# Performance work log

Hardware: AMD Instinct MI355X
Metric: run time of the kernel (lower is better)

The kernel has to match this reference:

```python
import jax, jax.numpy as jnp
import numpy as np

B, LQ, LK, D = 8, 1024, 4096, 1024


def setup_inputs() -> dict:
    key = jax.random.key(0)
    k1, k2, k3, k4, k5, k6 = jax.random.split(key, 6)
    s = 1.0 / np.sqrt(D)
    return {
        "T": jax.random.normal(k1, (B, LQ, D), dtype=jnp.float32),
        "S": jax.random.normal(k2, (B, LK, D), dtype=jnp.float32),
        "Wq": jax.random.uniform(k3, (D, D), jnp.float32, -s, s),
        "Wk": jax.random.uniform(k4, (D, D), jnp.float32, -s, s),
        "Wv": jax.random.uniform(k5, (D, D), jnp.float32, -s, s),
        "Wo": jax.random.uniform(k6, (D, D), jnp.float32, -s, s),
    }


def reference(T, S, Wq, Wk, Wv, Wo):
    # Linear layers: y = x @ W.T (torch nn.Linear convention), bias=False
    q = jnp.einsum('bqd,ed->bqe', T, Wq)          # [B, LQ, D]
    k = jnp.einsum('bkd,ed->bke', S, Wk)          # [B, LK, D]
    v = jnp.einsum('bkd,ed->bke', S, Wv)          # [B, LK, D]
    scale = jnp.asarray(D, q.dtype) ** -0.5        # hidden_dim ** -0.5 (single head)
    attn = jnp.einsum('bqe,bke->bqk', q, k) * scale  # [B, LQ, LK]
    attn = jax.nn.softmax(attn, axis=-1)
    out = jnp.einsum('bqk,bke->bqe', attn, v)      # [B, LQ, D]
    return jnp.einsum('bqe,fe->bqf', out, Wo)      # output projection
```

## Files before the change

kernel.cpp:

```cpp
#include <hip/hip_runtime.h>
#include <stdint.h>

typedef __bf16 bf16;
typedef __bf16 bf16x8 __attribute__((ext_vector_type(8)));
typedef float f32x4 __attribute__((ext_vector_type(4)));

__device__ __forceinline__ void gload_lds16(const void* g, void* l) {
    __builtin_amdgcn_global_load_lds(
        (const __attribute__((address_space(1))) unsigned int*)g,
        (__attribute__((address_space(3))) unsigned int*)l, 16, 0, 0);
}

#define BAR()    asm volatile("s_barrier" ::: "memory")
#define WAITV(N) asm volatile("s_waitcnt vmcnt(" #N ")" ::: "memory")

template<int OMODE>
__global__ __launch_bounds__(512, 2)
void gemm256(const bf16* __restrict__ A, const bf16* __restrict__ B,
             void* __restrict__ Cv, int K, int N,
             long batchA, long batchB, long batchC, float alpha,
             int nbx, int nby, int GC)
{
    __shared__ __align__(16) bf16 lds[2][4][8192];

    const int nwg  = gridDim.x;
    const int orig = blockIdx.x;
    const int q8   = nwg >> 3, r8 = nwg & 7;
    const int xcd  = orig & 7, lid = orig >> 3;
    const int p    = (xcd < r8 ? xcd * (q8 + 1) : r8 * (q8 + 1) + (xcd - r8) * q8) + lid;
    const int perb = nbx * nby;
    const int z    = p / perb;
    const int pb   = p - z * perb;
    const int sw   = nby * GC;
    const int st   = pb / sw;
    const int rem  = pb - st * sw;
    const int by   = rem / GC;
    const int bx   = st * GC + (rem - by * GC);

    const long rowb = (long)by << 8;
    const long colb = (long)bx << 8;

    const int t  = threadIdx.x;
    const int l  = t & 63;
    const int w  = t >> 6;
    const int wm = w >> 2;
    const int wn = w & 3;

    const int sL   = (t * 16) ^ (((t >> 3) & 3) << 4);
    const int srow = sL >> 6;
    const int sk   = (sL & 63) >> 1;
    const bf16* Ab = A + (long)z * batchA;
    const bf16* Bb = B + (long)z * batchB;
    const bf16* gA = Ab + (rowb + srow) * (long)K + sk;
    const bf16* gB = Bb + (colb + srow) * (long)K + sk;
    const long rstep = 128L * K;
    const int  d0 = t * 8, d1 = t * 8 + 4096;

    const int xl    = ((l >> 1) & 3) << 4;
    const int aBase = ((wm * 128 + (l & 15)) * 64 + ((l >> 4) << 4)) ^ xl;
    const int bBase = ((wn * 64  + (l & 15)) * 64 + ((l >> 4) << 4)) ^ xl;

    f32x4 acc[8][4] = {};
    bf16x8 av[4], bv[4];

#define STG(S, R, G, KOFF) do { \
    const bf16* _g = (G) + (KOFF); \
    gload_lds16(_g,         &lds[S][R][d0]); \
    gload_lds16(_g + rstep, &lds[S][R][d1]); \
  } while (0)

#define RD(S, R, OFF) (*(const bf16x8*)((const char*)&lds[S][R][0] + (OFF)))

#define MM(MB) \
    __builtin_amdgcn_s_setprio(1); \
    _Pragma("unroll") for (int mi = 0; mi < 4; ++mi) \
      _Pragma("unroll") for (int nj = 0; nj < 4; ++nj) \
        acc[MB + mi][nj] = __builtin_amdgcn_mfma_f32_16x16x32_bf16(av[mi], bv[nj], acc[MB + mi][nj], 0, 0, 0); \
    __builtin_amdgcn_s_setprio(0);

#define PH1(S, STGX) { \
    _Pragma("unroll") for (int nj = 0; nj < 4; ++nj) bv[nj] = RD(S, 2, bBase + nj * 1024); \
    _Pragma("unroll") for (int mi = 0; mi < 4; ++mi) av[mi] = RD(S, 0, aBase + mi * 1024); \
    STGX; BAR(); MM(0) BAR(); }

#define PH2(S, STGX) { \
    _Pragma("unroll") for (int mi = 0; mi < 4; ++mi) av[mi] = RD(S, 0, aBase + 4096 + mi * 1024); \
    STGX; BAR(); MM(4) BAR(); }

#define PH3(S, STGX) { \
    _Pragma("unroll") for (int nj = 0; nj < 4; ++nj) bv[nj] = RD(S, 3, bBase + nj * 1024); \
    _Pragma("unroll") for (int mi = 0; mi < 4; ++mi) av[mi] = RD(S, 1, aBase + mi * 1024); \
    STGX; BAR(); MM(0) BAR(); }

#define PH4(S, STGX, WT) { \
    _Pragma("unroll") for (int mi = 0; mi < 4; ++mi) av[mi] = RD(S, 1, aBase + 4096 + mi * 1024); \
    STGX; BAR(); MM(4) WT; BAR(); }

    STG(0, 0, gA, 0);
    STG(0, 1, gA, 32);
    STG(0, 2, gB, 0);
    STG(0, 3, gB, 32);
    STG(1, 2, gB, 64);
    STG(1, 0, gA, 64);
    STG(1, 3, gB, 96);
    WAITV(6);
    BAR();

    const int NI = K >> 7;
    for (int i = 0; i < NI - 1; ++i) {
        const int kb = i << 7;
        const int kn = kb + 128;
        PH1(0, STG(1, 1, gA, kb + 96));
        PH2(0, STG(0, 2, gB, kn));
        PH3(0, STG(0, 0, gA, kn));
        PH4(0, STG(0, 3, gB, kn + 32), WAITV(6));
        PH1(1, STG(0, 1, gA, kn + 32));
        PH2(1, STG(1, 2, gB, kn + 64));
        PH3(1, STG(1, 0, gA, kn + 64));
        PH4(1, STG(1, 3, gB, kn + 96), WAITV(6));
    }
    {
        const int kb = (NI - 1) << 7;
        PH1(0, STG(1, 1, gA, kb + 96));
        PH2(0, );
        PH3(0, );
        PH4(0, , WAITV(0));
        PH1(1, );
        PH2(1, );
        PH3(1, );
        PH4(1, , );
    }
#undef STG
#undef RD
#undef MM
#undef PH1
#undef PH2
#undef PH3
#undef PH4

    const int r0 = (l >> 4) << 2;

    if constexpr (OMODE == 2) {
        const long cb0 = colb + wn * 64 + (l & 15);
        const long rb0 = rowb + wm * 128 + r0;
#pragma unroll
        for (int mf = 0; mf < 8; ++mf)
#pragma unroll
          for (int nj = 0; nj < 4; ++nj) {
            const long col = cb0 + nj * 16;
#pragma unroll
            for (int r = 0; r < 4; ++r) {
                const long row = rb0 + mf * 16 + r;
                ((float*)Cv)[(long)z * batchC + row * (long)N + col] = acc[mf][nj][r] * alpha;
            }
          }
    } else {
        bf16* epi = &lds[0][0][0];
        const int rrow   = t >> 5;
        const int cchunk = (t & 31) << 3;
        const int myh = (OMODE == 0) ? wm : (wn >> 1);
#pragma unroll
        for (int h = 0; h < 2; ++h) {
            if (myh == h) {
#pragma unroll
                for (int mf = 0; mf < 8; ++mf)
#pragma unroll
                  for (int nj = 0; nj < 4; ++nj)
#pragma unroll
                    for (int r = 0; r < 4; ++r) {
                        const float v = acc[mf][nj][r] * alpha;
                        int orow = wm * 128 + mf * 16 + r0 + r;
                        int ocol = wn * 64 + nj * 16 + (l & 15);
                        if (OMODE == 1) { int tmp = orow; orow = ocol; ocol = tmp; }
                        epi[(orow - h * 128) * 280 + ocol] = (bf16)v;
                    }
            }
            __syncthreads();
#pragma unroll
            for (int pp = 0; pp < 8; ++pp) {
                const int lrow = pp * 16 + rrow;
                const int row  = h * 128 + lrow;
                uint4 d = *(const uint4*)&epi[lrow * 280 + cchunk];
                if (OMODE == 0) {
                    bf16* Cb = (bf16*)Cv + (long)z * batchC;
                    *(uint4*)&Cb[(rowb + row) * (long)N + colb + cchunk] = d;
                } else {
                    const long zz  = rowb >> 12;
                    const long lk0 = (rowb & 4095) + cchunk;
                    *(uint4*)&((bf16*)Cv)[zz * 4194304L + (colb + row) * 4096L + lk0] = d;
                }
            }
            __syncthreads();
        }
    }
}

__global__ void cvt_bf16(const float* __restrict__ in, bf16* __restrict__ out, long n8)
{
    const long stride = (long)gridDim.x * 256;
    for (long i = (long)blockIdx.x * 256 + threadIdx.x; i < n8; i += stride) {
        const float4* p = (const float4*)in + i * 2;
        float4 a = p[0], b = p[1];
        union { bf16 h[8]; uint4 u; } o;
        o.h[0] = (bf16)a.x; o.h[1] = (bf16)a.y; o.h[2] = (bf16)a.z; o.h[3] = (bf16)a.w;
        o.h[4] = (bf16)b.x; o.h[5] = (bf16)b.y; o.h[6] = (bf16)b.z; o.h[7] = (bf16)b.w;
        ((uint4*)out)[i] = o.u;
    }
}

__global__ __launch_bounds__(256)
void softmax_rows(bf16* __restrict__ P)
{
    const long base = (long)blockIdx.x * 4096;
    const int t = threadIdx.x;
    union U { uint4 u; bf16 h[8]; };
    U d0, d1;
    d0.u = *(const uint4*)&P[base + t * 8];
    d1.u = *(const uint4*)&P[base + 2048 + t * 8];
    float v[16];
#pragma unroll
    for (int i = 0; i < 8; ++i) { v[i] = (float)d0.h[i]; v[8 + i] = (float)d1.h[i]; }
    float mx = v[0];
#pragma unroll
    for (int i = 1; i < 16; ++i) mx = fmaxf(mx, v[i]);
    for (int o = 32; o; o >>= 1) mx = fmaxf(mx, __shfl_xor(mx, o));
    __shared__ float redm[4], reds[4];
    if ((t & 63) == 0) redm[t >> 6] = mx;
    __syncthreads();
    mx = fmaxf(fmaxf(redm[0], redm[1]), fmaxf(redm[2], redm[3]));
    float s = 0.f;
#pragma unroll
    for (int i = 0; i < 16; ++i) { v[i] = __expf(v[i] - mx); s += v[i]; }
    for (int o = 32; o; o >>= 1) s += __shfl_xor(s, o);
    if ((t & 63) == 0) reds[t >> 6] = s;
    __syncthreads();
    s = reds[0] + reds[1] + reds[2] + reds[3];
    const float inv = 1.f / s;
    U o0, o1;
#pragma unroll
    for (int i = 0; i < 8; ++i) {
        o0.h[i] = (bf16)(v[i] * inv);
        o1.h[i] = (bf16)(v[8 + i] * inv);
    }
    *(uint4*)&P[base + t * 8]        = o0.u;
    *(uint4*)&P[base + 2048 + t * 8] = o1.u;
}

extern "C" void kernel_launch(void* const* d_in, const int* in_sizes, int n_in,
                              void* d_out, int out_size, void* d_ws, size_t ws_size,
                              hipStream_t stream)
{
    (void)in_sizes; (void)n_in; (void)out_size; (void)ws_size;
    const float* T  = (const float*)d_in[0];
    const float* S  = (const float*)d_in[1];
    const float* Wq = (const float*)d_in[2];
    const float* Wk = (const float*)d_in[3];
    const float* Wv = (const float*)d_in[4];
    const float* Wo = (const float*)d_in[5];
    float* Y = (float*)d_out;
    char* ws = (char*)d_ws;

    bf16* Wqb = (bf16*)(ws + 0);
    bf16* Wkb = (bf16*)(ws + 2097152);
    bf16* Wvb = (bf16*)(ws + 4194304);
    bf16* Wob = (bf16*)(ws + 6291456);
    bf16* Tb  = (bf16*)(ws + 8388608);
    bf16* Ob  = Tb;
    bf16* Qb  = (bf16*)(ws + 25165824);
    bf16* Sb  = (bf16*)(ws + 41943040);
    bf16* Pb  = Sb;
    bf16* Kb  = (bf16*)(ws + 109051904);
    bf16* VTb = (bf16*)(ws + 176160768);

    cvt_bf16<<<512,   256, 0, stream>>>(Wq, Wqb, 131072);
    cvt_bf16<<<512,   256, 0, stream>>>(Wk, Wkb, 131072);
    cvt_bf16<<<512,   256, 0, stream>>>(Wv, Wvb, 131072);
    cvt_bf16<<<512,   256, 0, stream>>>(Wo, Wob, 131072);
    cvt_bf16<<<4096,  256, 0, stream>>>(T, Tb, 1048576);
    cvt_bf16<<<16384, 256, 0, stream>>>(S, Sb, 4194304);

    gemm256<0><<<128, 512, 0, stream>>>(Tb, Wqb, Qb, 1024, 1024, 0, 0, 0, 1.f, 4, 32, 4);
    gemm256<0><<<512, 512, 0, stream>>>(Sb, Wkb, Kb, 1024, 1024, 0, 0, 0, 1.f, 4, 128, 4);
    gemm256<1><<<512, 512, 0, stream>>>(Sb, Wvb, VTb, 1024, 1024, 0, 0, 0, 1.f, 4, 128, 4);

    gemm256<0><<<512, 512, 0, stream>>>(Qb, Kb, Pb, 1024, 4096,
        1024L * 1024, 4096L * 1024, 1024L * 4096, 0.03125f, 16, 4, 4);

    softmax_rows<<<8192, 256, 0, stream>>>(Pb);

    gemm256<0><<<128, 512, 0, stream>>>(Pb, VTb, Ob, 4096, 1024,
        1024L * 4096, 1024L * 4096, 1024L * 1024, 1.f, 4, 4, 4);

    gemm256<2><<<128, 512, 0, stream>>>(Ob, Wob, Y, 1024, 1024, 0, 0, 0, 1.f, 4, 32, 4);
}
```

Measured before the change: 448.3 us.

## Make GEMM persistent over two tiles, prefetching the next tile during the tail

Adds a tiles-per-block template parameter so each workgroup computes several consecutive 256x256 output tiles. The next tile's first K-slices are staged into LDS during the previous tile's final iterations, overlapping the pipeline fill with compute. The LDS-staged coalesced epilogue is replaced with direct scattered global stores from registers so LDS stays free for the prefetch. The K, V and QK^T launches switch to 256 blocks with two tiles each and a grouping factor of 1. The direct stores are uncoalesced, especially the transposed V store, and half as many blocks lowers parallelism.

```diff
diff --git a/kernel.cpp b/kernel.cpp
--- a/kernel.cpp
+++ b/kernel.cpp
@@ -14,7 +14,7 @@
 #define BAR()    asm volatile("s_barrier" ::: "memory")
 #define WAITV(N) asm volatile("s_waitcnt vmcnt(" #N ")" ::: "memory")
 
-template<int OMODE>
+template<int OMODE, int TPB>
 __global__ __launch_bounds__(512, 2)
 void gemm256(const bf16* __restrict__ A, const bf16* __restrict__ B,
              void* __restrict__ Cv, int K, int N,
@@ -28,17 +28,6 @@
     const int q8   = nwg >> 3, r8 = nwg & 7;
     const int xcd  = orig & 7, lid = orig >> 3;
     const int p    = (xcd < r8 ? xcd * (q8 + 1) : r8 * (q8 + 1) + (xcd - r8) * q8) + lid;
-    const int perb = nbx * nby;
-    const int z    = p / perb;
-    const int pb   = p - z * perb;
-    const int sw   = nby * GC;
-    const int st   = pb / sw;
-    const int rem  = pb - st * sw;
-    const int by   = rem / GC;
-    const int bx   = st * GC + (rem - by * GC);
-
-    const long rowb = (long)by << 8;
-    const long colb = (long)bx << 8;
 
     const int t  = threadIdx.x;
     const int l  = t & 63;
@@ -49,10 +38,6 @@
     const int sL   = (t * 16) ^ (((t >> 3) & 3) << 4);
     const int srow = sL >> 6;
     const int sk   = (sL & 63) >> 1;
-    const bf16* Ab = A + (long)z * batchA;
-    const bf16* Bb = B + (long)z * batchB;
-    const bf16* gA = Ab + (rowb + srow) * (long)K + sk;
-    const bf16* gB = Bb + (colb + srow) * (long)K + sk;
     const long rstep = 128L * K;
     const int  d0 = t * 8, d1 = t * 8 + 4096;
 
@@ -60,8 +45,10 @@
     const int aBase = ((wm * 128 + (l & 15)) * 64 + ((l >> 4) << 4)) ^ xl;
     const int bBase = ((wn * 64  + (l & 15)) * 64 + ((l >> 4) << 4)) ^ xl;
 
-    f32x4 acc[8][4] = {};
-    bf16x8 av[4], bv[4];
+    const int perb = nbx * nby;
+    const int sw   = nby * GC;
+    const int NI   = K >> 7;
+    const int r0   = (l >> 4) << 2;
 
 #define STG(S, R, G, KOFF) do { \
     const bf16* _g = (G) + (KOFF); \
@@ -96,39 +83,124 @@
     _Pragma("unroll") for (int mi = 0; mi < 4; ++mi) av[mi] = RD(S, 1, aBase + 4096 + mi * 1024); \
     STGX; BAR(); MM(4) WT; BAR(); }
 
-    STG(0, 0, gA, 0);
-    STG(0, 1, gA, 32);
-    STG(0, 2, gB, 0);
-    STG(0, 3, gB, 32);
-    STG(1, 2, gB, 64);
-    STG(1, 0, gA, 64);
-    STG(1, 3, gB, 96);
-    WAITV(6);
-    BAR();
-
-    const int NI = K >> 7;
-    for (int i = 0; i < NI - 1; ++i) {
-        const int kb = i << 7;
-        const int kn = kb + 128;
-        PH1(0, STG(1, 1, gA, kb + 96));
-        PH2(0, STG(0, 2, gB, kn));
-        PH3(0, STG(0, 0, gA, kn));
-        PH4(0, STG(0, 3, gB, kn + 32), WAITV(6));
-        PH1(1, STG(0, 1, gA, kn + 32));
-        PH2(1, STG(1, 2, gB, kn + 64));
-        PH3(1, STG(1, 0, gA, kn + 64));
-        PH4(1, STG(1, 3, gB, kn + 96), WAITV(6));
-    }
-    {
-        const int kb = (NI - 1) << 7;
-        PH1(0, STG(1, 1, gA, kb + 96));
-        PH2(0, );
-        PH3(0, );
-        PH4(0, , WAITV(0));
-        PH1(1, );
-        PH2(1, );
-        PH3(1, );
-        PH4(1, , );
+    for (int tt = 0; tt < TPB; ++tt) {
+        const int g   = p * TPB + tt;
+        const int z   = g / perb;
+        const int pb  = g - z * perb;
+        const int st  = pb / sw;
+        const int rem = pb - st * sw;
+        const int by  = rem / GC;
+        const int bx  = st * GC + (rem - by * GC);
+        const long rowb = (long)by << 8;
+        const long colb = (long)bx << 8;
+        const bf16* gA = A + (long)z * batchA + (rowb + srow) * (long)K + sk;
+        const bf16* gB = B + (long)z * batchB + (colb + srow) * (long)K + sk;
+
+        const bf16* gA2 = gA;
+        const bf16* gB2 = gB;
+        if (TPB > 1 && tt < TPB - 1) {
+            const int g2   = g + 1;
+            const int z2   = g2 / perb;
+            const int pb2  = g2 - z2 * perb;
+            const int st2  = pb2 / sw;
+            const int rem2 = pb2 - st2 * sw;
+            const int by2  = rem2 / GC;
+            const int bx2  = st2 * GC + (rem2 - by2 * GC);
+            gA2 = A + (long)z2 * batchA + (((long)by2 << 8) + srow) * (long)K + sk;
+            gB2 = B + (long)z2 * batchB + (((long)bx2 << 8) + srow) * (long)K + sk;
+        }
+
+        f32x4 acc[8][4] = {};
+        bf16x8 av[4], bv[4];
+
+        if (tt == 0) {
+            STG(0, 0, gA, 0);
+            STG(0, 1, gA, 32);
+            STG(0, 2, gB, 0);
+            STG(0, 3, gB, 32);
+            STG(1, 2, gB, 64);
+            STG(1, 0, gA, 64);
+            STG(1, 3, gB, 96);
+            WAITV(6);
+            BAR();
+        }
+
+        for (int i = 0; i < NI - 1; ++i) {
+            const int kb = i << 7;
+            const int kn = kb + 128;
+            PH1(0, STG(1, 1, gA, kb + 96));
+            PH2(0, STG(0, 2, gB, kn));
+            PH3(0, STG(0, 0, gA, kn));
+            PH4(0, STG(0, 3, gB, kn + 32), WAITV(6));
+            PH1(1, STG(0, 1, gA, kn + 32));
+            PH2(1, STG(1, 2, gB, kn + 64));
+            PH3(1, STG(1, 0, gA, kn + 64));
+            PH4(1, STG(1, 3, gB, kn + 96), WAITV(6));
+        }
+        {
+            const int kb = (NI - 1) << 7;
+            if (tt < TPB - 1) {
+                PH1(0, STG(1, 1, gA, kb + 96));
+                PH2(0, STG(0, 2, gB2, 0));
+                PH3(0, STG(0, 0, gA2, 0));
+                PH4(0, STG(0, 3, gB2, 32), WAITV(6));
+                PH1(1, STG(0, 1, gA2, 32));
+                PH2(1, STG(1, 2, gB2, 64));
+                PH3(1, STG(1, 0, gA2, 64));
+                PH4(1, STG(1, 3, gB2, 96), );
+            } else {
+                PH1(0, STG(1, 1, gA, kb + 96));
+                PH2(0, );
+                PH3(0, );
+                PH4(0, , WAITV(0));
+                PH1(1, );
+                PH2(1, );
+                PH3(1, );
+                PH4(1, , );
+            }
+        }
+
+        if constexpr (OMODE == 0) {
+            bf16* Cb = (bf16*)Cv + (long)z * batchC;
+            const long cb0 = colb + wn * 64 + (l & 15);
+            const long rb0 = rowb + wm * 128 + r0;
+#pragma unroll
+            for (int mf = 0; mf < 8; ++mf)
+#pragma unroll
+              for (int nj = 0; nj < 4; ++nj) {
+                const long col = cb0 + nj * 16;
+#pragma unroll
+                for (int r = 0; r < 4; ++r)
+                    Cb[(rb0 + mf * 16 + r) * (long)N + col] = (bf16)(acc[mf][nj][r] * alpha);
+              }
+        } else if constexpr (OMODE == 1) {
+            const long e0 = colb + wn * 64 + (l & 15);
+            const long rbase = rowb + wm * 128 + r0;
+#pragma unroll
+            for (int mf = 0; mf < 8; ++mf)
+#pragma unroll
+              for (int nj = 0; nj < 4; ++nj) {
+                const long row = rbase + mf * 16;
+                union { bf16 h[4]; uint2 u; } pk;
+#pragma unroll
+                for (int r = 0; r < 4; ++r) pk.h[r] = (bf16)(acc[mf][nj][r] * alpha);
+                *(uint2*)&((bf16*)Cv)[(row >> 12) * 4194304L + (e0 + nj * 16) * 4096L + (row & 4095)] = pk.u;
+              }
+        } else {
+            const long cb0 = colb + wn * 64 + (l & 15);
+            const long rb0 = rowb + wm * 128 + r0;
+#pragma unroll
+            for (int mf = 0; mf < 8; ++mf)
+#pragma unroll
+              for (int nj = 0; nj < 4; ++nj) {
+                const long col = cb0 + nj * 16;
+#pragma unroll
+                for (int r = 0; r < 4; ++r)
+                    ((float*)Cv)[(long)z * batchC + (rb0 + mf * 16 + r) * (long)N + col] = acc[mf][nj][r] * alpha;
+              }
+        }
+
+        if (TPB > 1 && tt < TPB - 1) { WAITV(6); BAR(); }
     }
 #undef STG
 #undef RD
@@ -137,62 +209,6 @@
 #undef PH2
 #undef PH3
 #undef PH4
-
-    const int r0 = (l >> 4) << 2;
-
-    if constexpr (OMODE == 2) {
-        const long cb0 = colb + wn * 64 + (l & 15);
-        const long rb0 = rowb + wm * 128 + r0;
-#pragma unroll
-        for (int mf = 0; mf < 8; ++mf)
-#pragma unroll
-          for (int nj = 0; nj < 4; ++nj) {
-            const long col = cb0 + nj * 16;
-#pragma unroll
-            for (int r = 0; r < 4; ++r) {
-                const long row = rb0 + mf * 16 + r;
-                ((float*)Cv)[(long)z * batchC + row * (long)N + col] = acc[mf][nj][r] * alpha;
-            }
-          }
-    } else {
-        bf16* epi = &lds[0][0][0];
-        const int rrow   = t >> 5;
-        const int cchunk = (t & 31) << 3;
-        const int myh = (OMODE == 0) ? wm : (wn >> 1);
-#pragma unroll
-        for (int h = 0; h < 2; ++h) {
-            if (myh == h) {
-#pragma unroll
-                for (int mf = 0; mf < 8; ++mf)
-#pragma unroll
-                  for (int nj = 0; nj < 4; ++nj)
-#pragma unroll
-                    for (int r = 0; r < 4; ++r) {
-                        const float v = acc[mf][nj][r] * alpha;
-                        int orow = wm * 128 + mf * 16 + r0 + r;
-                        int ocol = wn * 64 + nj * 16 + (l & 15);
-                        if (OMODE == 1) { int tmp = orow; orow = ocol; ocol = tmp; }
-                        epi[(orow - h * 128) * 280 + ocol] = (bf16)v;
-                    }
-            }
-            __syncthreads();
-#pragma unroll
-            for (int pp = 0; pp < 8; ++pp) {
-                const int lrow = pp * 16 + rrow;
-                const int row  = h * 128 + lrow;
-                uint4 d = *(const uint4*)&epi[lrow * 280 + cchunk];
-                if (OMODE == 0) {
-                    bf16* Cb = (bf16*)Cv + (long)z * batchC;
-                    *(uint4*)&Cb[(rowb + row) * (long)N + colb + cchunk] = d;
-                } else {
-                    const long zz  = rowb >> 12;
-                    const long lk0 = (rowb & 4095) + cchunk;
-                    *(uint4*)&((bf16*)Cv)[zz * 4194304L + (colb + row) * 4096L + lk0] = d;
-                }
-            }
-            __syncthreads();
-        }
-    }
 }
 
 __global__ void cvt_bf16(const float* __restrict__ in, bf16* __restrict__ out, long n8)
@@ -279,17 +295,17 @@
     cvt_bf16<<<4096,  256, 0, stream>>>(T, Tb, 1048576);
     cvt_bf16<<<16384, 256, 0, stream>>>(S, Sb, 4194304);
 
-    gemm256<0><<<128, 512, 0, stream>>>(Tb, Wqb, Qb, 1024, 1024, 0, 0, 0, 1.f, 4, 32, 4);
-    gemm256<0><<<512, 512, 0, stream>>>(Sb, Wkb, Kb, 1024, 1024, 0, 0, 0, 1.f, 4, 128, 4);
-    gemm256<1><<<512, 512, 0, stream>>>(Sb, Wvb, VTb, 1024, 1024, 0, 0, 0, 1.f, 4, 128, 4);
-
-    gemm256<0><<<512, 512, 0, stream>>>(Qb, Kb, Pb, 1024, 4096,
-        1024L * 1024, 4096L * 1024, 1024L * 4096, 0.03125f, 16, 4, 4);
+    gemm256<0,1><<<128, 512, 0, stream>>>(Tb, Wqb, Qb, 1024, 1024, 0, 0, 0, 1.f, 4, 32, 4);
+    gemm256<0,2><<<256, 512, 0, stream>>>(Sb, Wkb, Kb, 1024, 1024, 0, 0, 0, 1.f, 4, 128, 1);
+    gemm256<1,2><<<256, 512, 0, stream>>>(Sb, Wvb, VTb, 1024, 1024, 0, 0, 0, 1.f, 4, 128, 1);
+
+    gemm256<0,2><<<256, 512, 0, stream>>>(Qb, Kb, Pb, 1024, 4096,
+        1024L * 1024, 4096L * 1024, 1024L * 4096, 0.03125f, 16, 4, 1);
 
     softmax_rows<<<8192, 256, 0, stream>>>(Pb);
 
-    gemm256<0><<<128, 512, 0, stream>>>(Pb, VTb, Ob, 4096, 1024,
+    gemm256<0,1><<<128, 512, 0, stream>>>(Pb, VTb, Ob, 4096, 1024,
         1024L * 4096, 1024L * 4096, 1024L * 1024, 1.f, 4, 4, 4);
 
-    gemm256<2><<<128, 512, 0, stream>>>(Ob, Wob, Y, 1024, 1024, 0, 0, 0, 1.f, 4, 32, 4);
-}
+    gemm256<2,1><<<128, 512, 0, stream>>>(Ob, Wob, Y, 1024, 1024, 0, 0, 0, 1.f, 4, 32, 4);
+}
```

Measured after the change: 612.5 us. +36.6%, slower.
